# Optimization experiments

Hardware: AMD Instinct MI355X
Metric: run time of the kernel (lower is better)

Reference implementation:

```python
import jax, jax.numpy as jnp
import numpy as np

B, S, D, H = 2, 2048, 1024, 16
DK = D // H  # 64

def setup_inputs() -> dict:
    key = jax.random.key(0)
    ks = jax.random.split(key, 8)
    xavier = np.sqrt(6.0 / (D + D))  # xavier_uniform bound for square Linear
    def lin_w(k):
        return jax.random.uniform(k, (D, D), jnp.float32, -xavier, xavier)
    return {
        'Q': jax.random.normal(ks[0], (B, S, D), jnp.float32),
        'length': jax.random.randint(ks[1], (B,), 1, S + 1, jnp.int32),
        'Wq': lin_w(ks[2]), 'bq': jnp.zeros((D,), jnp.float32),
        'Wk': lin_w(ks[3]), 'bk': jnp.zeros((D,), jnp.float32),
        'Wv': lin_w(ks[4]), 'bv': jnp.zeros((D,), jnp.float32),
    }

def reference(Q, length, Wq, bq, Wk, bk, Wv, bv):
    # project and split heads: [B,S,D] -> [B,H,S,DK]
    def heads(x, W, b):
        y = jnp.einsum('bsd,de->bse', x, W) + b
        return y.reshape(B, S, H, DK).transpose(0, 2, 1, 3)
    q = heads(Q, Wq, bq)
    k = heads(Q, Wk, bk)
    v = heads(Q, Wv, bv)
    scores = jnp.einsum('bhqd,bhkd->bhqk', q, k) / np.sqrt(DK)
    scores = jnp.exp(scores)  # NOTE: raw exp, no max-subtraction (faithful)
    # multiplicative key mask: mask[b,k] = k < length[b], broadcast over q,h
    mask = (jnp.arange(S)[None, :] < length[:, None]).astype(scores.dtype)
    scores = scores * mask[:, None, None, :]
    attn = scores / (jnp.sum(scores, axis=-1, keepdims=True) + 1e-8)
    ctx = jnp.einsum('bhqk,bhkd->bhqd', attn, v)
    return ctx.transpose(0, 2, 1, 3).reshape(B, S, D)
```

## Files before the change

### kernel.cpp

```cpp
#include <hip/hip_runtime.h>
#include <hip/hip_bf16.h>

#define B_  2
#define S_  2048
#define D_  1024
#define H_  16
#define DK_ 64
#define M_  (B_ * S_)

typedef short short8 __attribute__((ext_vector_type(8)));
typedef float float4v __attribute__((ext_vector_type(4)));

#define QSCALE 0.18033688011112042f

static __device__ __forceinline__ ushort f32_to_bf16bits(float f) {
    union { __hip_bfloat16 h; ushort u; } cv;
    cv.h = __float2bfloat16(f);
    return cv.u;
}

static __device__ __forceinline__ void glds16(const ushort* g, ushort* l) {
    __builtin_amdgcn_global_load_lds(
        (const __attribute__((address_space(1))) unsigned int*)g,
        (__attribute__((address_space(3))) unsigned int*)l, 16, 0, 0);
}

__global__ __launch_bounds__(256) void prep(
    const float* __restrict__ X, const float* __restrict__ W0,
    const float* __restrict__ W1, const float* __restrict__ W2,
    ushort* __restrict__ Xb, ushort* __restrict__ Wt)
{
    const int z = blockIdx.z;
    const int t = threadIdx.x;

    if (z >= 3) {
        const int blk = (z - 3) * 256 + blockIdx.y * 16 + blockIdx.x;
        const int i = blk * 2048 + t * 8;
        float4v a = *(const float4v*)(X + i);
        float4v b = *(const float4v*)(X + i + 4);
        short8 o;
        o[0] = (short)f32_to_bf16bits(a[0]); o[1] = (short)f32_to_bf16bits(a[1]);
        o[2] = (short)f32_to_bf16bits(a[2]); o[3] = (short)f32_to_bf16bits(a[3]);
        o[4] = (short)f32_to_bf16bits(b[0]); o[5] = (short)f32_to_bf16bits(b[1]);
        o[6] = (short)f32_to_bf16bits(b[2]); o[7] = (short)f32_to_bf16bits(b[3]);
        *(short8*)(Xb + i) = o;
        return;
    }

    const float* W = (z == 0) ? W0 : ((z == 1) ? W1 : W2);
    ushort* out = Wt + (size_t)z * D_ * D_;

    __shared__ ushort tile[64 * 72];
    int n0 = blockIdx.x * 64, k0 = blockIdx.y * 64;
    int r = t >> 3, g = t & 7;

    #pragma unroll
    for (int p = 0; p < 2; ++p) {
        int rr = r + p * 32;
        const float* src = W + (size_t)(k0 + rr) * D_ + n0 + g * 8;
        float4v a = *(const float4v*)src;
        float4v b = *(const float4v*)(src + 4);
        short8 o;
        o[0] = (short)f32_to_bf16bits(a[0]); o[1] = (short)f32_to_bf16bits(a[1]);
        o[2] = (short)f32_to_bf16bits(a[2]); o[3] = (short)f32_to_bf16bits(a[3]);
        o[4] = (short)f32_to_bf16bits(b[0]); o[5] = (short)f32_to_bf16bits(b[1]);
        o[6] = (short)f32_to_bf16bits(b[2]); o[7] = (short)f32_to_bf16bits(b[3]);
        *(short8*)&tile[rr * 72 + g * 8] = o;
    }
    __syncthreads();
    #pragma unroll
    for (int p = 0; p < 2; ++p) {
        int rr = r + p * 32;
        short8 v;
        #pragma unroll
        for (int i = 0; i < 8; ++i)
            v[i] = (short)tile[(g * 8 + i) * 72 + rr];
        *(short8*)(out + (size_t)(n0 + rr) * D_ + k0 + g * 8) = v;
    }
}

__global__ __launch_bounds__(256, 2) void proj_gemm(
    const ushort* __restrict__ X,
    const ushort* __restrict__ Wt,
    const float* __restrict__ b0, const float* __restrict__ b1,
    const float* __restrict__ b2,
    const int* __restrict__ length,
    ushort* __restrict__ qkv)
{
    const int m0 = blockIdx.x * 64, n0 = blockIdx.y * 128;
    const int bidx = m0 >> 11;
    const int s0 = m0 & (S_ - 1);
    const bool kv = (s0 < length[bidx]);

    __shared__ __align__(16) ushort As[64 * 64];
    __shared__ __align__(16) ushort Bs[3][128 * 64];

    const int t = threadIdx.x;
    const int lane = t & 63, wid = t >> 6;
    const int quad = lane >> 4, l16 = lane & 15;
    const int wr = wid >> 1, wc = wid & 1;

    float4v accq[2][4] = {}, acck[2][4] = {}, accv[2][4] = {};

    for (int kt = 0; kt < 16; ++kt) {
        const int k0 = kt * 64;
        __syncthreads();
        #pragma unroll
        for (int j = 0; j < 2; ++j) {
            const int cid = wid * 128 + j * 64 + lane;
            const int row = cid >> 3;
            const int cl  = (cid & 7) ^ (row & 7);
            glds16(X + (size_t)(m0 + row) * D_ + k0 + cl * 8, &As[cid * 8]);
        }
        #pragma unroll
        for (int j = 0; j < 4; ++j) {
            const int cid = wid * 256 + j * 64 + lane;
            const int row = cid >> 3;
            const int cl  = (cid & 7) ^ (row & 7);
            const size_t off = (size_t)(n0 + row) * D_ + k0 + cl * 8;
            glds16(Wt + off, &Bs[0][cid * 8]);
            if (kv) {
                glds16(Wt + (size_t)D_ * D_ + off,     &Bs[1][cid * 8]);
                glds16(Wt + (size_t)2 * D_ * D_ + off, &Bs[2][cid * 8]);
            }
        }
        __syncthreads();

        #pragma unroll
        for (int ks = 0; ks < 2; ++ks) {
            short8 a[2];
            #pragma unroll
            for (int i = 0; i < 2; ++i) {
                const int r = wr * 32 + i * 16 + l16;
                const int ph = (ks * 4 + quad) ^ (r & 7);
                a[i] = *(short8*)&As[r * 64 + ph * 8];
            }
            short8 bq[4];
            #pragma unroll
            for (int j = 0; j < 4; ++j) {
                const int r = wc * 64 + j * 16 + l16;
                const int ph = (ks * 4 + quad) ^ (r & 7);
                bq[j] = *(short8*)&Bs[0][r * 64 + ph * 8];
            }
            #pragma unroll
            for (int i = 0; i < 2; ++i)
                #pragma unroll
                for (int j = 0; j < 4; ++j)
                    accq[i][j] = __builtin_amdgcn_mfma_f32_16x16x32_bf16(
                        a[i], bq[j], accq[i][j], 0, 0, 0);
            if (kv) {
                short8 bk[4], bv[4];
                #pragma unroll
                for (int j = 0; j < 4; ++j) {
                    const int r = wc * 64 + j * 16 + l16;
                    const int ph = (ks * 4 + quad) ^ (r & 7);
                    bk[j] = *(short8*)&Bs[1][r * 64 + ph * 8];
                    bv[j] = *(short8*)&Bs[2][r * 64 + ph * 8];
                }
                #pragma unroll
                for (int i = 0; i < 2; ++i)
                    #pragma unroll
                    for (int j = 0; j < 4; ++j) {
                        acck[i][j] = __builtin_amdgcn_mfma_f32_16x16x32_bf16(
                            a[i], bk[j], acck[i][j], 0, 0, 0);
                        accv[i][j] = __builtin_amdgcn_mfma_f32_16x16x32_bf16(
                            a[i], bv[j], accv[i][j], 0, 0, 0);
                    }
            }
        }
    }

    #pragma unroll
    for (int j = 0; j < 4; ++j) {
        const int col = n0 + wc * 64 + j * 16 + l16;
        const int h = col >> 6, dk = col & (DK_ - 1);
        const float bvq = b0[col], bvk = b1[col], bvv = b2[col];
        #pragma unroll
        for (int i = 0; i < 2; ++i) {
            #pragma unroll
            for (int rr = 0; rr < 4; ++rr) {
                const int row = m0 + wr * 32 + i * 16 + quad * 4 + rr;
                const int s = row & (S_ - 1);
                const size_t hdr = ((size_t)(bidx * H_ + h) * S_ + s) * DK_ + dk;
                qkv[hdr] = f32_to_bf16bits((accq[i][j][rr] + bvq) * QSCALE);
                if (kv) {
                    qkv[(size_t)M_ * D_ + hdr] =
                        f32_to_bf16bits(acck[i][j][rr] + bvk);
                    qkv[(size_t)2 * M_ * D_ +
                        ((size_t)(bidx * H_ + h) * DK_ + dk) * S_ + s] =
                        f32_to_bf16bits(accv[i][j][rr] + bvv);
                }
            }
        }
    }
}

__global__ __launch_bounds__(256, 3) void attention(
    const ushort* __restrict__ qkv, const int* __restrict__ length,
    float* __restrict__ out)
{
    const int b = blockIdx.z, h = blockIdx.y, q0 = blockIdx.x * 64;
    int len = length[b];
    if (len > S_) len = S_;
    if (len < 1) len = 1;
    const int nkt = (len + 63) >> 6;

    const ushort* qb = qkv + ((size_t)(b * H_ + h) * S_ + q0) * DK_;
    const ushort* kb = qkv + (size_t)M_ * D_ + (size_t)(b * H_ + h) * S_ * DK_;
    const ushort* vb = qkv + (size_t)2 * M_ * D_ + (size_t)(b * H_ + h) * DK_ * S_;

    __shared__ __align__(16) ushort Qs[64 * 64];
    __shared__ __align__(16) ushort Ks[2][64 * 64];
    __shared__ __align__(16) ushort Vs[2][64 * 64];
    __shared__ __align__(16) ushort Ps[64 * 64];

    const int t = threadIdx.x, lane = t & 63, wid = t >> 6;
    const int quad = lane >> 4, l16 = lane & 15;
    const int qrow = wid * 16 + l16;
    const int e8 = (l16 & 7) << 1;

    #pragma unroll
    for (int j = 0; j < 2; ++j) {
        const int cid = wid * 128 + j * 64 + lane;
        const int row = cid >> 3;
        const int cl  = (cid & 7) ^ (row & 7);
        glds16(qb + (size_t)row * DK_ + cl * 8, &Qs[cid * 8]);
        glds16(kb + (size_t)row * DK_ + cl * 8, &Ks[0][cid * 8]);
        glds16(vb + (size_t)row * S_ + cl * 8,  &Vs[0][cid * 8]);
    }
    __syncthreads();

    short8 qfrag[2];
    #pragma unroll
    for (int ks = 0; ks < 2; ++ks) {
        const int phb = (ks * 4 + quad) ^ (l16 & 7);
        qfrag[ks] = *(short8*)&Qs[qrow * 64 + phb * 8];
    }

    short8 ones8;
    #pragma unroll
    for (int i = 0; i < 8; ++i) ones8[i] = (short)0x3F80;

    float4v cacc[4] = {};
    float4v racc = {};

    for (int kt = 0; kt < nkt; ++kt) {
        const int cur = kt & 1, nxt = cur ^ 1;
        if (kt + 1 < nkt) {
            #pragma unroll
            for (int j = 0; j < 2; ++j) {
                const int cid = wid * 128 + j * 64 + lane;
                const int row = cid >> 3;
                const int cl  = (cid & 7) ^ (row & 7);
                glds16(kb + (size_t)((kt + 1) * 64 + row) * DK_ + cl * 8,
                       &Ks[nxt][cid * 8]);
                glds16(vb + (size_t)row * S_ + (kt + 1) * 64 + cl * 8,
                       &Vs[nxt][cid * 8]);
            }
        }

        float4v sacc[4] = {};
        #pragma unroll
        for (int ks = 0; ks < 2; ++ks) {
            #pragma unroll
            for (int ct = 0; ct < 4; ++ct) {
                const int krow = ct * 16 + l16;
                const int pha = (ks * 4 + quad) ^ (krow & 7);
                short8 ak = *(short8*)&Ks[cur][krow * 64 + pha * 8];
                sacc[ct] = __builtin_amdgcn_mfma_f32_16x16x32_bf16(
                    ak, qfrag[ks], sacc[ct], 0, 0, 0);
            }
        }

        const bool full = ((kt + 1) * 64 <= len);
        #pragma unroll
        for (int ct = 0; ct < 4; ++ct) {
            float v0 = __builtin_amdgcn_exp2f(sacc[ct][0]);
            float v1 = __builtin_amdgcn_exp2f(sacc[ct][1]);
            float v2 = __builtin_amdgcn_exp2f(sacc[ct][2]);
            float v3 = __builtin_amdgcn_exp2f(sacc[ct][3]);
            if (!full) {
                const int kb0 = kt * 64 + ct * 16 + quad * 4;
                v0 = (kb0 + 0 < len) ? v0 : 0.f;
                v1 = (kb0 + 1 < len) ? v1 : 0.f;
                v2 = (kb0 + 2 < len) ? v2 : 0.f;
                v3 = (kb0 + 3 < len) ? v3 : 0.f;
            }
            uint2 w;
            w.x = (__float_as_uint(v0) >> 16) | (__float_as_uint(v1) & 0xFFFF0000u);
            w.y = (__float_as_uint(v2) >> 16) | (__float_as_uint(v3) & 0xFFFF0000u);
            const int c8 = (ct * 4 + quad) ^ e8;
            *(uint2*)&Ps[qrow * 64 + c8 * 4] = w;
        }

        #pragma unroll
        for (int ks = 0; ks < 2; ++ks) {
            const int pp = ((ks * 4 + quad) * 2) ^ e8;
            short8 ap = *(short8*)&Ps[qrow * 64 + pp * 4];
            #pragma unroll
            for (int ct = 0; ct < 4; ++ct) {
                const int vrow = ct * 16 + l16;
                const int phv = (ks * 4 + quad) ^ (vrow & 7);
                short8 vv = *(short8*)&Vs[cur][vrow * 64 + phv * 8];
                cacc[ct] = __builtin_amdgcn_mfma_f32_16x16x32_bf16(
                    ap, vv, cacc[ct], 0, 0, 0);
            }
            racc = __builtin_amdgcn_mfma_f32_16x16x32_bf16(
                ap, ones8, racc, 0, 0, 0);
        }
        __syncthreads();
    }

    #pragma unroll
    for (int rr = 0; rr < 4; ++rr) {
        const float inv = 1.0f / (racc[rr] + 1e-8f);
        const int q = q0 + wid * 16 + quad * 4 + rr;
        #pragma unroll
        for (int ct = 0; ct < 4; ++ct) {
            const int d = h * 64 + ct * 16 + l16;
            out[((size_t)b * S_ + q) * D_ + d] = cacc[ct][rr] * inv;
        }
    }
}

extern "C" void kernel_launch(void* const* d_in, const int* in_sizes, int n_in,
                              void* d_out, int out_size, void* d_ws, size_t ws_size,
                              hipStream_t stream)
{
    const float* Q   = (const float*)d_in[0];
    const int*   len = (const int*)d_in[1];
    const float* Wq  = (const float*)d_in[2];
    const float* bq  = (const float*)d_in[3];
    const float* Wk  = (const float*)d_in[4];
    const float* bk  = (const float*)d_in[5];
    const float* Wv  = (const float*)d_in[6];
    const float* bv  = (const float*)d_in[7];
    float* out = (float*)d_out;

    ushort* ws  = (ushort*)d_ws;
    ushort* Xb  = ws;
    ushort* Wt  = ws + (size_t)M_ * D_;
    ushort* qkv = Wt + (size_t)3 * D_ * D_;

    dim3 gPr(16, 16, 11);
    prep<<<gPr, 256, 0, stream>>>(Q, Wq, Wk, Wv, Xb, Wt);

    dim3 gP(M_ / 64, D_ / 128);
    proj_gemm<<<gP, 256, 0, stream>>>(Xb, Wt, bq, bk, bv, len, qkv);

    dim3 gA(S_ / 64, H_, B_);
    attention<<<gA, 256, 0, stream>>>(qkv, len, out);
}
```

Baseline: 155.7 us.

## Process 128 query rows per attention block, reusing K/V tiles across two query tiles

Each attention workgroup now handles 128 query rows instead of 64, with each wave computing two 16-row query tiles against the same K and V fragments. This halves the K/V tile loads from global memory and LDS per query row. The Q buffer is reused as the P staging area to save shared memory. The trade-off is fewer workgroups (half the grid), more registers per thread and lower occupancy (launch bounds lowered to 2 blocks per CU).

```diff
diff --git a/kernel.cpp b/kernel.cpp
--- a/kernel.cpp
+++ b/kernel.cpp
@@ -195,11 +195,11 @@
     }
 }
 
-__global__ __launch_bounds__(256, 3) void attention(
+__global__ __launch_bounds__(256, 2) void attention(
     const ushort* __restrict__ qkv, const int* __restrict__ length,
     float* __restrict__ out)
 {
-    const int b = blockIdx.z, h = blockIdx.y, q0 = blockIdx.x * 64;
+    const int b = blockIdx.z, h = blockIdx.y, q0 = blockIdx.x * 128;
     int len = length[b];
     if (len > S_) len = S_;
     if (len < 1) len = 1;
@@ -209,40 +209,47 @@
     const ushort* kb = qkv + (size_t)M_ * D_ + (size_t)(b * H_ + h) * S_ * DK_;
     const ushort* vb = qkv + (size_t)2 * M_ * D_ + (size_t)(b * H_ + h) * DK_ * S_;
 
-    __shared__ __align__(16) ushort Qs[64 * 64];
+    __shared__ __align__(16) ushort QPs[128 * 64];
     __shared__ __align__(16) ushort Ks[2][64 * 64];
     __shared__ __align__(16) ushort Vs[2][64 * 64];
-    __shared__ __align__(16) ushort Ps[64 * 64];
 
     const int t = threadIdx.x, lane = t & 63, wid = t >> 6;
     const int quad = lane >> 4, l16 = lane & 15;
-    const int qrow = wid * 16 + l16;
     const int e8 = (l16 & 7) << 1;
 
+    #pragma unroll
+    for (int j = 0; j < 4; ++j) {
+        const int cid = wid * 256 + j * 64 + lane;
+        const int row = cid >> 3;
+        const int cl  = (cid & 7) ^ (row & 7);
+        glds16(qb + (size_t)row * DK_ + cl * 8, &QPs[cid * 8]);
+    }
     #pragma unroll
     for (int j = 0; j < 2; ++j) {
         const int cid = wid * 128 + j * 64 + lane;
         const int row = cid >> 3;
         const int cl  = (cid & 7) ^ (row & 7);
-        glds16(qb + (size_t)row * DK_ + cl * 8, &Qs[cid * 8]);
         glds16(kb + (size_t)row * DK_ + cl * 8, &Ks[0][cid * 8]);
         glds16(vb + (size_t)row * S_ + cl * 8,  &Vs[0][cid * 8]);
     }
     __syncthreads();
 
-    short8 qfrag[2];
-    #pragma unroll
-    for (int ks = 0; ks < 2; ++ks) {
-        const int phb = (ks * 4 + quad) ^ (l16 & 7);
-        qfrag[ks] = *(short8*)&Qs[qrow * 64 + phb * 8];
-    }
+    short8 qfrag[2][2];
+    #pragma unroll
+    for (int qt = 0; qt < 2; ++qt)
+        #pragma unroll
+        for (int ks = 0; ks < 2; ++ks) {
+            const int qrow = wid * 32 + qt * 16 + l16;
+            const int phb = (ks * 4 + quad) ^ (l16 & 7);
+            qfrag[qt][ks] = *(short8*)&QPs[qrow * 64 + phb * 8];
+        }
 
     short8 ones8;
     #pragma unroll
     for (int i = 0; i < 8; ++i) ones8[i] = (short)0x3F80;
 
-    float4v cacc[4] = {};
-    float4v racc = {};
+    float4v cacc[2][4] = {};
+    float4v racc[2] = {};
 
     for (int kt = 0; kt < nkt; ++kt) {
         const int cur = kt & 1, nxt = cur ^ 1;
@@ -259,66 +266,80 @@
             }
         }
 
-        float4v sacc[4] = {};
+        float4v sacc[2][4] = {};
         #pragma unroll
         for (int ks = 0; ks < 2; ++ks) {
             #pragma unroll
             for (int ct = 0; ct < 4; ++ct) {
                 const int krow = ct * 16 + l16;
-                const int pha = (ks * 4 + quad) ^ (krow & 7);
+                const int pha = (ks * 4 + quad) ^ (l16 & 7);
                 short8 ak = *(short8*)&Ks[cur][krow * 64 + pha * 8];
-                sacc[ct] = __builtin_amdgcn_mfma_f32_16x16x32_bf16(
-                    ak, qfrag[ks], sacc[ct], 0, 0, 0);
+                sacc[0][ct] = __builtin_amdgcn_mfma_f32_16x16x32_bf16(
+                    ak, qfrag[0][ks], sacc[0][ct], 0, 0, 0);
+                sacc[1][ct] = __builtin_amdgcn_mfma_f32_16x16x32_bf16(
+                    ak, qfrag[1][ks], sacc[1][ct], 0, 0, 0);
             }
         }
 
         const bool full = ((kt + 1) * 64 <= len);
         #pragma unroll
-        for (int ct = 0; ct < 4; ++ct) {
-            float v0 = __builtin_amdgcn_exp2f(sacc[ct][0]);
-            float v1 = __builtin_amdgcn_exp2f(sacc[ct][1]);
-            float v2 = __builtin_amdgcn_exp2f(sacc[ct][2]);
-            float v3 = __builtin_amdgcn_exp2f(sacc[ct][3]);
-            if (!full) {
-                const int kb0 = kt * 64 + ct * 16 + quad * 4;
-                v0 = (kb0 + 0 < len) ? v0 : 0.f;
-                v1 = (kb0 + 1 < len) ? v1 : 0.f;
-                v2 = (kb0 + 2 < len) ? v2 : 0.f;
-                v3 = (kb0 + 3 < len) ? v3 : 0.f;
-            }
-            uint2 w;
-            w.x = (__float_as_uint(v0) >> 16) | (__float_as_uint(v1) & 0xFFFF0000u);
-            w.y = (__float_as_uint(v2) >> 16) | (__float_as_uint(v3) & 0xFFFF0000u);
-            const int c8 = (ct * 4 + quad) ^ e8;
-            *(uint2*)&Ps[qrow * 64 + c8 * 4] = w;
+        for (int qt = 0; qt < 2; ++qt) {
+            const int prow = wid * 32 + qt * 16 + l16;
+            #pragma unroll
+            for (int ct = 0; ct < 4; ++ct) {
+                float v0 = __builtin_amdgcn_exp2f(sacc[qt][ct][0]);
+                float v1 = __builtin_amdgcn_exp2f(sacc[qt][ct][1]);
+                float v2 = __builtin_amdgcn_exp2f(sacc[qt][ct][2]);
+                float v3 = __builtin_amdgcn_exp2f(sacc[qt][ct][3]);
+                if (!full) {
+                    const int kb0 = kt * 64 + ct * 16 + quad * 4;
+                    v0 = (kb0 + 0 < len) ? v0 : 0.f;
+                    v1 = (kb0 + 1 < len) ? v1 : 0.f;
+                    v2 = (kb0 + 2 < len) ? v2 : 0.f;
+                    v3 = (kb0 + 3 < len) ? v3 : 0.f;
+                }
+                uint2 w;
+                w.x = (__float_as_uint(v0) >> 16) | (__float_as_uint(v1) & 0xFFFF0000u);
+                w.y = (__float_as_uint(v2) >> 16) | (__float_as_uint(v3) & 0xFFFF0000u);
+                const int c8 = (ct * 4 + quad) ^ e8;
+                *(uint2*)&QPs[prow * 64 + c8 * 4] = w;
+            }
         }
 
         #pragma unroll
         for (int ks = 0; ks < 2; ++ks) {
             const int pp = ((ks * 4 + quad) * 2) ^ e8;
-            short8 ap = *(short8*)&Ps[qrow * 64 + pp * 4];
+            short8 ap0 = *(short8*)&QPs[(wid * 32 + l16) * 64 + pp * 4];
+            short8 ap1 = *(short8*)&QPs[(wid * 32 + 16 + l16) * 64 + pp * 4];
             #pragma unroll
             for (int ct = 0; ct < 4; ++ct) {
                 const int vrow = ct * 16 + l16;
-                const int phv = (ks * 4 + quad) ^ (vrow & 7);
+                const int phv = (ks * 4 + quad) ^ (l16 & 7);
                 short8 vv = *(short8*)&Vs[cur][vrow * 64 + phv * 8];
-                cacc[ct] = __builtin_amdgcn_mfma_f32_16x16x32_bf16(
-                    ap, vv, cacc[ct], 0, 0, 0);
-            }
-            racc = __builtin_amdgcn_mfma_f32_16x16x32_bf16(
-                ap, ones8, racc, 0, 0, 0);
+                cacc[0][ct] = __builtin_amdgcn_mfma_f32_16x16x32_bf16(
+                    ap0, vv, cacc[0][ct], 0, 0, 0);
+                cacc[1][ct] = __builtin_amdgcn_mfma_f32_16x16x32_bf16(
+                    ap1, vv, cacc[1][ct], 0, 0, 0);
+            }
+            racc[0] = __builtin_amdgcn_mfma_f32_16x16x32_bf16(
+                ap0, ones8, racc[0], 0, 0, 0);
+            racc[1] = __builtin_amdgcn_mfma_f32_16x16x32_bf16(
+                ap1, ones8, racc[1], 0, 0, 0);
         }
         __syncthreads();
     }
 
     #pragma unroll
-    for (int rr = 0; rr < 4; ++rr) {
-        const float inv = 1.0f / (racc[rr] + 1e-8f);
-        const int q = q0 + wid * 16 + quad * 4 + rr;
-        #pragma unroll
-        for (int ct = 0; ct < 4; ++ct) {
-            const int d = h * 64 + ct * 16 + l16;
-            out[((size_t)b * S_ + q) * D_ + d] = cacc[ct][rr] * inv;
+    for (int qt = 0; qt < 2; ++qt) {
+        #pragma unroll
+        for (int rr = 0; rr < 4; ++rr) {
+            const float inv = 1.0f / (racc[qt][rr] + 1e-8f);
+            const int q = q0 + wid * 32 + qt * 16 + quad * 4 + rr;
+            #pragma unroll
+            for (int ct = 0; ct < 4; ++ct) {
+                const int d = h * 64 + ct * 16 + l16;
+                out[((size_t)b * S_ + q) * D_ + d] = cacc[qt][ct][rr] * inv;
+            }
         }
     }
 }
@@ -348,6 +369,6 @@
     dim3 gP(M_ / 64, D_ / 128);
     proj_gemm<<<gP, 256, 0, stream>>>(Xb, Wt, bq, bk, bv, len, qkv);
 
-    dim3 gA(S_ / 64, H_, B_);
+    dim3 gA(S_ / 128, H_, B_);
     attention<<<gA, 256, 0, stream>>>(qkv, len, out);
 }
```

Measured after the change: 162.0 us. 4.0% more time.
